# Kernel tuning notes

Hardware: AMD Instinct MI355X
Metric: run time of the kernel (lower is better)

Reference implementation:

```python
import jax, jax.numpy as jnp
import numpy as np

B, T, D = 2, 2048, 1024
NH, NKV, HD = 16, 4, 64
ROPE = 16  # partial RoPE dims (first 16 of 64)
HALF = ROPE // 2


def apply_rope(x, cos, sin):
    # x: (B, nH, T, HD); rotate first ROPE dims, pass the rest through
    x1 = x[..., :HALF]
    x2 = x[..., HALF:ROPE]
    xp = x[..., ROPE:]
    c = cos[None, None, :, :]  # (1,1,T,HALF)
    s = sin[None, None, :, :]
    return jnp.concatenate([x1 * c - x2 * s, x1 * s + x2 * c, xp], axis=-1)


def setup_inputs() -> dict:
    key = jax.random.key(0)
    k0, k1, k2 = jax.random.split(key, 3)
    x = jax.random.normal(k0, (B, T, D), dtype=jnp.float32)
    # RoPE tables for the rotated sub-dimension (half = ROPE//2 = 8)
    inv_freq = 1.0 / (10000.0 ** (jnp.arange(HALF, dtype=jnp.float32) / HALF))
    ang = jnp.arange(T, dtype=jnp.float32)[:, None] * inv_freq[None, :]
    cos = jnp.cos(ang)
    sin = jnp.sin(ang)
    attn_mask = jnp.tril(jnp.ones((T, T), dtype=bool))  # causal
    w_qkv = jax.random.normal(k1, ((NH + 2 * NKV) * HD, D), dtype=jnp.float32) * (D ** -0.5)
    w_out = jax.random.normal(k2, (D, D), dtype=jnp.float32) * (D ** -0.5)
    q_scale = jnp.full((NH, 1), 1.5, dtype=jnp.float32)
    k_scale = jnp.full((NKV, 1), 1.5, dtype=jnp.float32)
    return {"x": x, "cos": cos, "sin": sin, "attn_mask": attn_mask,
            "w_qkv": w_qkv, "w_out": w_out, "q_scale": q_scale, "k_scale": k_scale}


def reference(x, cos, sin, attn_mask, w_qkv, w_out, q_scale, k_scale):
    Bx, Tx, C = x.shape
    groups = NH // NKV
    qkv = x @ w_qkv.T  # (B,T,(NH+2*NKV)*HD)
    q, k, v = jnp.split(qkv, [NH * HD, (NH + NKV) * HD], axis=-1)
    q = q.reshape(Bx, Tx, NH, HD).transpose(0, 2, 1, 3)    # (B,NH,T,HD)
    k = k.reshape(Bx, Tx, NKV, HD).transpose(0, 2, 1, 3)   # (B,NKV,T,HD)
    v = v.reshape(Bx, Tx, NKV, HD).transpose(0, 2, 1, 3)
    # per-head qk gain scaling
    q = q * q_scale[None, :, :, None]  # (1,NH,1,1)
    k = k * k_scale[None, :, :, None]
    # partial RoPE on q and k
    q = apply_rope(q, cos[:Tx], sin[:Tx])
    k = apply_rope(k, cos[:Tx], sin[:Tx])
    # GQA expand (repeat_interleave along heads)
    ke = jnp.repeat(k, groups, axis=1)  # (B,NH,T,HD)
    ve = jnp.repeat(v, groups, axis=1)
    # scaled dot-product attention with causal mask
    scores = jnp.einsum('bhqd,bhkd->bhqk', q, ke) * (HD ** -0.5)
    scores = jnp.where(attn_mask[None, None], scores, -jnp.inf)
    probs = jax.nn.softmax(scores, axis=-1)
    ao = jnp.einsum('bhqk,bhkd->bhqd', probs, ve)  # (B,NH,T,HD)
    # xsa: subtract self-component along the (shared) kv value direction
    ao_r = ao.reshape(Bx, NKV, groups, Tx, HD)
    vv = v[:, :, None]  # (B,NKV,1,T,HD), broadcasts over groups
    dots = jnp.sum(ao_r * vv, axis=-1, keepdims=True)
    norm = jnp.maximum(jnp.sum(vv * vv, axis=-1, keepdims=True), 1e-8)
    ao = (ao_r - (dots / norm) * vv).reshape(Bx, NH, Tx, HD)
    out = ao.transpose(0, 2, 1, 3).reshape(Bx, Tx, C) @ w_out.T
    return out
```

## Files before the change

kernel.cpp:

```cpp
#include <hip/hip_runtime.h>
#include <hip/hip_bf16.h>

#define NB 2
#define NT 2048
#define ND 1024
#define NHEADS 16
#define NKVH 4
#define HDIM 64
#define QKVD 1536

typedef __attribute__((ext_vector_type(8))) short short8;
typedef __attribute__((ext_vector_type(4))) float floatx4;

#if defined(__has_builtin)
#  if __has_builtin(__builtin_amdgcn_global_load_lds)
#    define HAS_GLL 1
#  endif
#endif
#ifndef HAS_GLL
#  define HAS_GLL 0
#endif

__device__ __forceinline__ void gll16(const void* g, void* l, int lane) {
#if HAS_GLL
  (void)lane;
  __builtin_amdgcn_global_load_lds(
      (const __attribute__((address_space(1))) unsigned int*)g,
      (__attribute__((address_space(3))) unsigned int*)l, 16, 0, 0);
#else
  *(short8*)((short*)l) = *(const short8*)g;
#endif
}

__device__ __forceinline__ unsigned short f2bf(float f) {
  union { float f; unsigned int u; } cv; cv.f = f;
  unsigned int u = cv.u;
  u += 0x7fffu + ((u >> 16) & 1u);
  return (unsigned short)(u >> 16);
}
__device__ __forceinline__ float bf2f(unsigned short u) {
  union { unsigned int u; float f; } cv; cv.u = ((unsigned int)u) << 16; return cv.f;
}

__global__ __launch_bounds__(256) void cvt_bf16(const float* __restrict__ in,
                                                unsigned short* __restrict__ out,
                                                int n4) {
  int i = blockIdx.x * 256 + threadIdx.x;
  if (i < n4) {
    float4 v = ((const float4*)in)[i];
    ushort4 o;
    o.x = f2bf(v.x); o.y = f2bf(v.y); o.z = f2bf(v.z); o.w = f2bf(v.w);
    ((ushort4*)out)[i] = o;
  }
}

__global__ __launch_bounds__(256) void gemm_lds(
    const unsigned short* __restrict__ A,
    const unsigned short* __restrict__ Bm,
    float* __restrict__ C, int M, int N, int K)
{
  __shared__ __align__(16) short As[2][128][32];
  __shared__ __align__(16) short Bs[2][128][32];

  const int tid = threadIdx.x;
  const int wid = tid >> 6, lane = tid & 63;
  const int quad = lane >> 4, l16 = lane & 15;
  const int wm = (wid >> 1) * 64, wn = (wid & 1) * 64;
  const int m0 = blockIdx.x * 128, n0 = blockIdx.y * 128;

  const int r0 = tid >> 2;
  const int lc = ((tid & 3) ^ (r0 & 3)) * 8;

  const unsigned short* ag0 = A  + (size_t)(m0 + r0) * K + lc;
  const unsigned short* ag1 = ag0 + (size_t)64 * K;
  const unsigned short* bg0 = Bm + (size_t)(n0 + r0) * K + lc;
  const unsigned short* bg1 = bg0 + (size_t)64 * K;

  short* asb = &As[0][0][0];
  short* bsb = &Bs[0][0][0];
  const int lofs = (HAS_GLL ? wid * 512 : tid * 8);

  const int cs = (quad ^ (l16 & 3)) * 8;

  floatx4 acc[4][4] = {};

  gll16(ag0, asb + lofs, lane);
  gll16(ag1, asb + 2048 + lofs, lane);
  gll16(bg0, bsb + lofs, lane);
  gll16(bg1, bsb + 2048 + lofs, lane);

  const int NIT = K / 32;
  for (int it = 0; it < NIT; it++) {
    __syncthreads();
    const int bi = it & 1, bn = bi ^ 1;
    if (it + 1 < NIT) {
      const int k = (it + 1) * 32;
      gll16(ag0 + k, asb + bn * 4096 + lofs, lane);
      gll16(ag1 + k, asb + bn * 4096 + 2048 + lofs, lane);
      gll16(bg0 + k, bsb + bn * 4096 + lofs, lane);
      gll16(bg1 + k, bsb + bn * 4096 + 2048 + lofs, lane);
    }

    short8 af[4], bf[4];
#pragma unroll
    for (int mi = 0; mi < 4; mi++) af[mi] = *(const short8*)&As[bi][wm + mi * 16 + l16][cs];
#pragma unroll
    for (int ni = 0; ni < 4; ni++) bf[ni] = *(const short8*)&Bs[bi][wn + ni * 16 + l16][cs];
#pragma unroll
    for (int mi = 0; mi < 4; mi++)
#pragma unroll
      for (int ni = 0; ni < 4; ni++)
        acc[mi][ni] = __builtin_amdgcn_mfma_f32_16x16x32_bf16(af[mi], bf[ni], acc[mi][ni], 0, 0, 0);
  }

#pragma unroll
  for (int mi = 0; mi < 4; mi++)
#pragma unroll
    for (int ni = 0; ni < 4; ni++)
#pragma unroll
      for (int r = 0; r < 4; r++) {
        int m = m0 + wm + mi * 16 + quad * 4 + r;
        int n = n0 + wn + ni * 16 + l16;
        C[(size_t)m * N + n] = acc[mi][ni][r];
      }
}

__global__ __launch_bounds__(256) void rope_pack(
    const float* __restrict__ qkv,
    const float* __restrict__ cosT, const float* __restrict__ sinT,
    const float* __restrict__ q_scale, const float* __restrict__ k_scale,
    unsigned short* __restrict__ qb, unsigned short* __restrict__ kb)
{
  const int b  = blockIdx.z;
  const int hh = blockIdx.y * 4 + (threadIdx.x >> 6);
  const int d  = threadIdx.x & 63;

  float scale; int soff; unsigned short* dbase;
  if (hh < NHEADS) {
    scale = q_scale[hh] * (0.125f * 1.44269504088896f);
    soff = hh * HDIM;
    dbase = qb + ((size_t)(b * NHEADS + hh) * NT) * HDIM;
  } else {
    int kvh = hh - NHEADS;
    scale = k_scale[kvh];
    soff = NHEADS * HDIM + kvh * HDIM;
    dbase = kb + ((size_t)(b * NKVH + kvh) * NT) * HDIM;
  }

  for (int i = 0; i < 8; i++) {
    const int t = blockIdx.x * 8 + i;
    const float* src = qkv + ((size_t)(b * NT + t)) * QKVD + soff;
    float out;
    if (d < 8) {
      float x1 = src[d], x2 = src[d + 8];
      float c = cosT[t * 8 + d], s = sinT[t * 8 + d];
      out = (x1 * c - x2 * s) * scale;
    } else if (d < 16) {
      float x1 = src[d - 8], x2 = src[d];
      float c = cosT[t * 8 + d - 8], s = sinT[t * 8 + d - 8];
      out = (x1 * s + x2 * c) * scale;
    } else {
      out = src[d] * scale;
    }
    dbase[(size_t)t * HDIM + d] = f2bf(out);
  }
}

__global__ __launch_bounds__(256) void vT(const float* __restrict__ qkv,
                                          unsigned short* __restrict__ vtb)
{
  const int tt  = blockIdx.x;
  const int kvh = blockIdx.y;
  const int b   = blockIdx.z;
  const int tid = threadIdx.x;

  __shared__ float tile[64][65];

  {
    const int tl = tid >> 2, d0 = (tid & 3) * 16;
    const float* src = qkv + ((size_t)(b * NT + tt * 64 + tl)) * QKVD
                       + (NHEADS + NKVH) * HDIM + kvh * HDIM + d0;
#pragma unroll
    for (int j = 0; j < 16; j += 4) {
      float4 v = *(const float4*)(src + j);
      tile[tl][d0 + j + 0] = v.x; tile[tl][d0 + j + 1] = v.y;
      tile[tl][d0 + j + 2] = v.z; tile[tl][d0 + j + 3] = v.w;
    }
  }
  __syncthreads();
  {
    const int dd = tid >> 2, t0 = (tid & 3) * 16;
    unsigned short* dst = vtb + ((size_t)((b * NKVH + kvh) * HDIM + dd)) * NT + tt * 64 + t0;
#pragma unroll
    for (int j = 0; j < 16; j++) dst[j] = f2bf(tile[t0 + j][dd]);
  }
}

__global__ __launch_bounds__(256) void fattn(
    const unsigned short* __restrict__ qb,
    const unsigned short* __restrict__ kb,
    const unsigned short* __restrict__ vtb,
    unsigned short* __restrict__ aob,
    float* __restrict__ pbuf)
{
  const int idx = blockIdx.x;
  const int h = blockIdx.y, b = blockIdx.z;
  const int kv = h >> 2;

  int qt, j0, cnt, chunk; bool direct;
  if (idx < 16) { qt = 16 + idx; j0 = 0; cnt = 16; chunk = 0; direct = false; }
  else {
    int rel = idx - 16, s = 16 - (rel >> 1);
    if ((rel & 1) == 0) { qt = s - 1;  j0 = 0;  cnt = s; chunk = 0; direct = true;  }
    else                { qt = s + 15; j0 = 16; cnt = s; chunk = 1; direct = false; }
  }

  const int tid = threadIdx.x;
  const int wid = tid >> 6, lane = tid & 63;
  const int quad = lane >> 4, l16 = lane & 15;
  const int hi8 = l16 >> 3, lo8 = l16 & 7;

  __shared__ __align__(16) short Ks[2][64][64];
  __shared__ __align__(16) short Vs[2][64][64];
  __shared__ __align__(16) short Ps[4][16][64];

  const unsigned short* qg = qb + ((size_t)((b * NHEADS + h) * NT + qt * 64)) * HDIM;
  const int qrow = wid * 16 + l16;
  short8 aq0 = *(const short8*)(qg + (size_t)qrow * HDIM + quad * 8);
  short8 aq1 = *(const short8*)(qg + (size_t)qrow * HDIM + 32 + quad * 8);

  const int sr  = tid >> 3;
  const int lck = ((tid & 7) ^ (sr & 7)) * 8;
  const unsigned short* kgp0 = kb  + ((size_t)((b * NKVH + kv) * NT) + sr) * HDIM + lck;
  const unsigned short* vgp0 = vtb + ((size_t)((b * NKVH + kv) * HDIM) + sr) * NT + lck;
  short* ksb = &Ks[0][0][0];
  short* vsb = &Vs[0][0][0];
  const int lofs = (HAS_GLL ? wid * 512 : tid * 8);

  const int cs0 = (quad ^ lo8) * 8;
  const int cs1 = cs0 ^ 32;

  int pwo[4][4];
#pragma unroll
  for (int r = 0; r < 4; r++) {
    const int row = quad * 4 + r;
#pragma unroll
    for (int nb = 0; nb < 4; nb++)
      pwo[r][nb] = wid * 1024 + row * 64 + (((nb * 2 + hi8) ^ (row & 7)) * 8) + lo8;
  }
  short* psf = &Ps[0][0][0];

  floatx4 acc_o[4] = {};
  float lsum[4] = {0.f, 0.f, 0.f, 0.f};

  {
    const unsigned short* kg = kgp0 + (size_t)j0 * 64 * HDIM;
    const unsigned short* vg = vgp0 + j0 * 64;
    gll16(kg, ksb + lofs, lane);
    gll16(kg + 32 * HDIM, ksb + 2048 + lofs, lane);
    gll16(vg, vsb + lofs, lane);
    gll16(vg + (size_t)32 * NT, vsb + 2048 + lofs, lane);
  }

  for (int i = 0; i < cnt; i++) {
    const int jt = j0 + i;
    __syncthreads();
    const int bi = i & 1, bn = bi ^ 1;
    if (i + 1 < cnt) {
      const unsigned short* kg = kgp0 + (size_t)(jt + 1) * 64 * HDIM;
      const unsigned short* vg = vgp0 + (jt + 1) * 64;
      gll16(kg, ksb + bn * 4096 + lofs, lane);
      gll16(kg + 32 * HDIM, ksb + bn * 4096 + 2048 + lofs, lane);
      gll16(vg, vsb + bn * 4096 + lofs, lane);
      gll16(vg + (size_t)32 * NT, vsb + bn * 4096 + 2048 + lofs, lane);
    }

    floatx4 s[4] = {};
#pragma unroll
    for (int nb = 0; nb < 4; nb++) {
      short8 bk0 = *(const short8*)&Ks[bi][nb * 16 + l16][cs0];
      short8 bk1 = *(const short8*)&Ks[bi][nb * 16 + l16][cs1];
      s[nb] = __builtin_amdgcn_mfma_f32_16x16x32_bf16(aq0, bk0, s[nb], 0, 0, 0);
      s[nb] = __builtin_amdgcn_mfma_f32_16x16x32_bf16(aq1, bk1, s[nb], 0, 0, 0);
    }

    if (jt == qt) {
#pragma unroll
      for (int nb = 0; nb < 4; nb++) {
        int col = nb * 16 + l16;
#pragma unroll
        for (int r = 0; r < 4; r++)
          if (col > wid * 16 + quad * 4 + r) s[nb][r] = -INFINITY;
      }
    }

#pragma unroll
    for (int r = 0; r < 4; r++) {
#pragma unroll
      for (int nb = 0; nb < 4; nb++) {
        float p = __builtin_amdgcn_exp2f(s[nb][r]);
        lsum[r] += p;
        psf[pwo[r][nb]] = (short)(__float_as_uint(p) >> 16);
      }
    }

    short8 ap0 = *(const short8*)&Ps[wid][l16][cs0];
    short8 ap1 = *(const short8*)&Ps[wid][l16][cs1];
#pragma unroll
    for (int nb = 0; nb < 4; nb++) {
      short8 bv0 = *(const short8*)&Vs[bi][nb * 16 + l16][cs0];
      short8 bv1 = *(const short8*)&Vs[bi][nb * 16 + l16][cs1];
      acc_o[nb] = __builtin_amdgcn_mfma_f32_16x16x32_bf16(ap0, bv0, acc_o[nb], 0, 0, 0);
      acc_o[nb] = __builtin_amdgcn_mfma_f32_16x16x32_bf16(ap1, bv1, acc_o[nb], 0, 0, 0);
    }
  }

  const int bl = (cnt - 1) & 1;

  if (direct) {
#pragma unroll
    for (int r = 0; r < 4; r++) {
      float ls = lsum[r];
#pragma unroll
      for (int off = 1; off < 16; off <<= 1) ls += __shfl_xor(ls, off);
      const float invl = 1.f / ls;

      const int rowl = wid * 16 + quad * 4 + r;
      const int vcol = ((rowl >> 3) ^ lo8) * 8 + (rowl & 7);
      float vd[4], dot = 0.f, vv = 0.f;
#pragma unroll
      for (int nb = 0; nb < 4; nb++) {
        vd[nb] = bf2f((unsigned short)Vs[bl][nb * 16 + l16][vcol]);
        dot += acc_o[nb][r] * invl * vd[nb];
        vv  += vd[nb] * vd[nb];
      }
#pragma unroll
      for (int off = 1; off < 16; off <<= 1) {
        dot += __shfl_xor(dot, off);
        vv  += __shfl_xor(vv, off);
      }
      const float coef = dot / fmaxf(vv, 1e-8f);
      unsigned short* dst = aob + ((size_t)(b * NT + qt * 64 + rowl)) * ND + h * HDIM + l16;
#pragma unroll
      for (int nb = 0; nb < 4; nb++)
        dst[nb * 16] = f2bf(acc_o[nb][r] * invl - coef * vd[nb]);
    }
  } else {
    const int slot = ((b * NHEADS + h) * 16 + (qt - 16)) * 2 + chunk;
    float* pO = pbuf + (size_t)slot * 4160;
    float* pl = pO + 4096;
#pragma unroll
    for (int r = 0; r < 4; r++) {
      float ls = lsum[r];
#pragma unroll
      for (int off = 1; off < 16; off <<= 1) ls += __shfl_xor(ls, off);
      const int rowl = wid * 16 + quad * 4 + r;
      if (l16 == 0) pl[rowl] = ls;
#pragma unroll
      for (int nb = 0; nb < 4; nb++)
        pO[rowl * 64 + nb * 16 + l16] = acc_o[nb][r];
    }
  }
}

__global__ __launch_bounds__(256) void redn(
    const float* __restrict__ pbuf,
    const unsigned short* __restrict__ vtb,
    unsigned short* __restrict__ aob)
{
  const int qt = 16 + blockIdx.x;
  const int h = blockIdx.y, b = blockIdx.z;
  const int kv = h >> 2;
  const int tid = threadIdx.x;

  const int slot0 = ((b * NHEADS + h) * 16 + blockIdx.x) * 2;
  const float* O0 = pbuf + (size_t)slot0 * 4160;
  const float* O1 = O0 + 4160;
  const float* l0 = O0 + 4096;
  const float* l1 = O1 + 4096;

  __shared__ short vt[64][66];

  {
    const int d = tid >> 2, tq = (tid & 3) * 16;
    const unsigned short* src = vtb + ((size_t)((b * NKVH + kv) * HDIM + d)) * NT + qt * 64 + tq;
    short8 v0 = *(const short8*)src;
    short8 v1 = *(const short8*)(src + 8);
    *(short8*)&vt[d][tq] = v0;
    *(short8*)&vt[d][tq + 8] = v1;
  }
  __syncthreads();

  const int row = tid >> 2, dq = tid & 3;
  const float invl = 1.f / (l0[row] + l1[row]);

  float o[16], vd[16];
  float dot = 0.f, vv = 0.f;
#pragma unroll
  for (int j = 0; j < 16; j++) {
    const int d = dq * 16 + j;
    float ov = (O0[row * 64 + d] + O1[row * 64 + d]) * invl;
    float v  = bf2f((unsigned short)vt[d][row]);
    o[j] = ov; vd[j] = v;
    dot += ov * v; vv += v * v;
  }
  dot += __shfl_xor(dot, 1); dot += __shfl_xor(dot, 2);
  vv  += __shfl_xor(vv, 1);  vv  += __shfl_xor(vv, 2);
  const float coef = dot / fmaxf(vv, 1e-8f);

  unsigned short* dst = aob + ((size_t)(b * NT + qt * 64 + row)) * ND + h * HDIM + dq * 16;
  ushort4 w0, w1, w2, w3;
  w0.x = f2bf(o[0] - coef * vd[0]);  w0.y = f2bf(o[1] - coef * vd[1]);
  w0.z = f2bf(o[2] - coef * vd[2]);  w0.w = f2bf(o[3] - coef * vd[3]);
  w1.x = f2bf(o[4] - coef * vd[4]);  w1.y = f2bf(o[5] - coef * vd[5]);
  w1.z = f2bf(o[6] - coef * vd[6]);  w1.w = f2bf(o[7] - coef * vd[7]);
  w2.x = f2bf(o[8] - coef * vd[8]);  w2.y = f2bf(o[9] - coef * vd[9]);
  w2.z = f2bf(o[10] - coef * vd[10]); w2.w = f2bf(o[11] - coef * vd[11]);
  w3.x = f2bf(o[12] - coef * vd[12]); w3.y = f2bf(o[13] - coef * vd[13]);
  w3.z = f2bf(o[14] - coef * vd[14]); w3.w = f2bf(o[15] - coef * vd[15]);
  ((ushort4*)dst)[0] = w0; ((ushort4*)dst)[1] = w1;
  ((ushort4*)dst)[2] = w2; ((ushort4*)dst)[3] = w3;
}

extern "C" void kernel_launch(void* const* d_in, const int* in_sizes, int n_in,
                              void* d_out, int out_size, void* d_ws, size_t ws_size,
                              hipStream_t stream) {
  const float* x       = (const float*)d_in[0];
  const float* cosT    = (const float*)d_in[1];
  const float* sinT    = (const float*)d_in[2];
  const float* w_qkv   = (const float*)d_in[4];
  const float* w_out   = (const float*)d_in[5];
  const float* q_scale = (const float*)d_in[6];
  const float* k_scale = (const float*)d_in[7];
  float* out = (float*)d_out;

  char* ws = (char*)d_ws;
  unsigned short* xb    = (unsigned short*)ws;
  unsigned short* qb    = xb;
  unsigned short* wqkvb = (unsigned short*)(ws + 8388608);
  unsigned short* kb    = wqkvb;
  unsigned short* woutb = (unsigned short*)(ws + 11534336);
  float*          qkv   = (float*)(ws + 13631488);
  float*          pbuf  = qkv;
  unsigned short* vtb   = (unsigned short*)(ws + 38797312);
  unsigned short* aob   = (unsigned short*)(ws + 40894464);

  cvt_bf16<<<(NB * NT * ND / 4 + 255) / 256, 256, 0, stream>>>(x, xb, NB * NT * ND / 4);
  cvt_bf16<<<(QKVD * ND / 4 + 255) / 256, 256, 0, stream>>>(w_qkv, wqkvb, QKVD * ND / 4);
  cvt_bf16<<<(ND * ND / 4 + 255) / 256, 256, 0, stream>>>(w_out, woutb, ND * ND / 4);

  gemm_lds<<<dim3(NB * NT / 128, QKVD / 128), 256, 0, stream>>>(
      xb, wqkvb, qkv, NB * NT, QKVD, ND);

  rope_pack<<<dim3(NT / 8, 5, NB), 256, 0, stream>>>(qkv, cosT, sinT, q_scale, k_scale, qb, kb);
  vT<<<dim3(NT / 64, NKVH, NB), 256, 0, stream>>>(qkv, vtb);

  fattn<<<dim3(48, NHEADS, NB), 256, 0, stream>>>(qb, kb, vtb, aob, pbuf);
  redn<<<dim3(16, NHEADS, NB), 256, 0, stream>>>(pbuf, vtb, aob);

  gemm_lds<<<dim3(NB * NT / 128, ND / 128), 256, 0, stream>>>(
      aob, woutb, out, NB * NT, ND, ND);
}
```

Measured before the change: 216.2 us.

## Fuse RoPE, scaling, bf16 pack and V transpose into QKV GEMM epilogue

The three fp32-to-bf16 conversion launches become a single kernel, and the QKV GEMM now applies the head scales, partial RoPE (exchanging rotate pairs through a lane shuffle), bf16 conversion and the V transpose directly in its epilogue. This drops the fp32 qkv intermediate round trip through memory and removes the rope_pack and vT launches. The workspace layout is reorganised to match. The cost is an epilogue with scattered 2-byte stores for Q/K and strided ushort4 stores for V^T, which may coalesce worse than the old dedicated kernels.

Result: faster. 195.2 us (-9.7%).

```diff
diff --git a/kernel.cpp b/kernel.cpp
--- a/kernel.cpp
+++ b/kernel.cpp
@@ -42,29 +42,41 @@
   union { unsigned int u; float f; } cv; cv.u = ((unsigned int)u) << 16; return cv.f;
 }
 
-__global__ __launch_bounds__(256) void cvt_bf16(const float* __restrict__ in,
-                                                unsigned short* __restrict__ out,
-                                                int n4) {
+#define N4_X   1048576
+#define N4_WQ   393216
+#define N4_WO   262144
+__global__ __launch_bounds__(256) void cvt_all(
+    const float* __restrict__ x, const float* __restrict__ wq,
+    const float* __restrict__ wo,
+    unsigned short* __restrict__ xb, unsigned short* __restrict__ wqb,
+    unsigned short* __restrict__ wob) {
   int i = blockIdx.x * 256 + threadIdx.x;
-  if (i < n4) {
-    float4 v = ((const float4*)in)[i];
-    ushort4 o;
-    o.x = f2bf(v.x); o.y = f2bf(v.y); o.z = f2bf(v.z); o.w = f2bf(v.w);
-    ((ushort4*)out)[i] = o;
-  }
-}
-
-__global__ __launch_bounds__(256) void gemm_lds(
+  const float* src; unsigned short* dst; int j;
+  if (i < N4_X)              { src = x;  dst = xb;  j = i; }
+  else if (i < N4_X + N4_WQ) { src = wq; dst = wqb; j = i - N4_X; }
+  else                       { src = wo; dst = wob; j = i - N4_X - N4_WQ; }
+  float4 v = ((const float4*)src)[j];
+  ushort4 o;
+  o.x = f2bf(v.x); o.y = f2bf(v.y); o.z = f2bf(v.z); o.w = f2bf(v.w);
+  ((ushort4*)dst)[j] = o;
+}
+
+__global__ __launch_bounds__(256) void gemm_qkv(
     const unsigned short* __restrict__ A,
     const unsigned short* __restrict__ Bm,
-    float* __restrict__ C, int M, int N, int K)
+    const float* __restrict__ cosT, const float* __restrict__ sinT,
+    const float* __restrict__ q_scale, const float* __restrict__ k_scale,
+    unsigned short* __restrict__ qb, unsigned short* __restrict__ kb,
+    unsigned short* __restrict__ vtb)
 {
+  const int M = NB * NT, N = QKVD, K = ND;
   __shared__ __align__(16) short As[2][128][32];
   __shared__ __align__(16) short Bs[2][128][32];
 
   const int tid = threadIdx.x;
   const int wid = tid >> 6, lane = tid & 63;
   const int quad = lane >> 4, l16 = lane & 15;
+  const int lo8 = l16 & 7;
   const int wm = (wid >> 1) * 64, wn = (wid & 1) * 64;
   const int m0 = blockIdx.x * 128, n0 = blockIdx.y * 128;
 
@@ -79,7 +91,6 @@
   short* asb = &As[0][0][0];
   short* bsb = &Bs[0][0][0];
   const int lofs = (HAS_GLL ? wid * 512 : tid * 8);
-
   const int cs = (quad ^ (l16 & 3)) * 8;
 
   floatx4 acc[4][4] = {};
@@ -100,7 +111,107 @@
       gll16(bg0 + k, bsb + bn * 4096 + lofs, lane);
       gll16(bg1 + k, bsb + bn * 4096 + 2048 + lofs, lane);
     }
-
+    short8 af[4], bf[4];
+#pragma unroll
+    for (int mi = 0; mi < 4; mi++) af[mi] = *(const short8*)&As[bi][wm + mi * 16 + l16][cs];
+#pragma unroll
+    for (int ni = 0; ni < 4; ni++) bf[ni] = *(const short8*)&Bs[bi][wn + ni * 16 + l16][cs];
+#pragma unroll
+    for (int mi = 0; mi < 4; mi++)
+#pragma unroll
+      for (int ni = 0; ni < 4; ni++)
+        acc[mi][ni] = __builtin_amdgcn_mfma_f32_16x16x32_bf16(af[mi], bf[ni], acc[mi][ni], 0, 0, 0);
+  }
+
+  const int hh = blockIdx.y * 2 + (wid & 1);
+
+  if (hh >= NHEADS + NKVH) {
+    const int kvh = hh - (NHEADS + NKVH);
+#pragma unroll
+    for (int mi = 0; mi < 4; mi++) {
+      const int mrow = m0 + wm + mi * 16 + quad * 4;
+      const int bb = mrow >> 11, tt = mrow & (NT - 1);
+#pragma unroll
+      for (int ni = 0; ni < 4; ni++) {
+        const int d = ni * 16 + l16;
+        ushort4 w;
+        w.x = f2bf(acc[mi][ni][0]); w.y = f2bf(acc[mi][ni][1]);
+        w.z = f2bf(acc[mi][ni][2]); w.w = f2bf(acc[mi][ni][3]);
+        *(ushort4*)(vtb + ((size_t)((bb * NKVH + kvh) * HDIM + d)) * NT + tt) = w;
+      }
+    }
+  } else {
+    float scl; unsigned short* dst0; int hloc;
+    if (hh < NHEADS) { scl = q_scale[hh] * (0.125f * 1.44269504088896f); hloc = hh; dst0 = qb; }
+    else             { scl = k_scale[hh - NHEADS];                        hloc = hh - NHEADS; dst0 = kb; }
+    const int nh = (hh < NHEADS) ? NHEADS : NKVH;
+#pragma unroll
+    for (int mi = 0; mi < 4; mi++) {
+#pragma unroll
+      for (int r = 0; r < 4; r++) {
+        const int mrow = m0 + wm + mi * 16 + quad * 4 + r;
+        const int bb = mrow >> 11, tt = mrow & (NT - 1);
+        unsigned short* drow = dst0 + ((size_t)((bb * nh + hloc) * NT + tt)) * HDIM;
+
+        const float own = acc[mi][0][r];
+        const float oth = __shfl_xor(own, 8);
+        const float c = cosT[tt * 8 + lo8], s = sinT[tt * 8 + lo8];
+        const float roped = (l16 < 8) ? (own * c - oth * s)
+                                      : (oth * s + own * c);
+        drow[l16] = f2bf(roped * scl);
+#pragma unroll
+        for (int ni = 1; ni < 4; ni++)
+          drow[ni * 16 + l16] = f2bf(acc[mi][ni][r] * scl);
+      }
+    }
+  }
+}
+
+__global__ __launch_bounds__(256) void gemm_lds(
+    const unsigned short* __restrict__ A,
+    const unsigned short* __restrict__ Bm,
+    float* __restrict__ C, int M, int N, int K)
+{
+  __shared__ __align__(16) short As[2][128][32];
+  __shared__ __align__(16) short Bs[2][128][32];
+
+  const int tid = threadIdx.x;
+  const int wid = tid >> 6, lane = tid & 63;
+  const int quad = lane >> 4, l16 = lane & 15;
+  const int wm = (wid >> 1) * 64, wn = (wid & 1) * 64;
+  const int m0 = blockIdx.x * 128, n0 = blockIdx.y * 128;
+
+  const int r0 = tid >> 2;
+  const int lc = ((tid & 3) ^ (r0 & 3)) * 8;
+
+  const unsigned short* ag0 = A  + (size_t)(m0 + r0) * K + lc;
+  const unsigned short* ag1 = ag0 + (size_t)64 * K;
+  const unsigned short* bg0 = Bm + (size_t)(n0 + r0) * K + lc;
+  const unsigned short* bg1 = bg0 + (size_t)64 * K;
+
+  short* asb = &As[0][0][0];
+  short* bsb = &Bs[0][0][0];
+  const int lofs = (HAS_GLL ? wid * 512 : tid * 8);
+  const int cs = (quad ^ (l16 & 3)) * 8;
+
+  floatx4 acc[4][4] = {};
+
+  gll16(ag0, asb + lofs, lane);
+  gll16(ag1, asb + 2048 + lofs, lane);
+  gll16(bg0, bsb + lofs, lane);
+  gll16(bg1, bsb + 2048 + lofs, lane);
+
+  const int NIT = K / 32;
+  for (int it = 0; it < NIT; it++) {
+    __syncthreads();
+    const int bi = it & 1, bn = bi ^ 1;
+    if (it + 1 < NIT) {
+      const int k = (it + 1) * 32;
+      gll16(ag0 + k, asb + bn * 4096 + lofs, lane);
+      gll16(ag1 + k, asb + bn * 4096 + 2048 + lofs, lane);
+      gll16(bg0 + k, bsb + bn * 4096 + lofs, lane);
+      gll16(bg1 + k, bsb + bn * 4096 + 2048 + lofs, lane);
+    }
     short8 af[4], bf[4];
 #pragma unroll
     for (int mi = 0; mi < 4; mi++) af[mi] = *(const short8*)&As[bi][wm + mi * 16 + l16][cs];
@@ -123,77 +234,6 @@
         int n = n0 + wn + ni * 16 + l16;
         C[(size_t)m * N + n] = acc[mi][ni][r];
       }
-}
-
-__global__ __launch_bounds__(256) void rope_pack(
-    const float* __restrict__ qkv,
-    const float* __restrict__ cosT, const float* __restrict__ sinT,
-    const float* __restrict__ q_scale, const float* __restrict__ k_scale,
-    unsigned short* __restrict__ qb, unsigned short* __restrict__ kb)
-{
-  const int b  = blockIdx.z;
-  const int hh = blockIdx.y * 4 + (threadIdx.x >> 6);
-  const int d  = threadIdx.x & 63;
-
-  float scale; int soff; unsigned short* dbase;
-  if (hh < NHEADS) {
-    scale = q_scale[hh] * (0.125f * 1.44269504088896f);
-    soff = hh * HDIM;
-    dbase = qb + ((size_t)(b * NHEADS + hh) * NT) * HDIM;
-  } else {
-    int kvh = hh - NHEADS;
-    scale = k_scale[kvh];
-    soff = NHEADS * HDIM + kvh * HDIM;
-    dbase = kb + ((size_t)(b * NKVH + kvh) * NT) * HDIM;
-  }
-
-  for (int i = 0; i < 8; i++) {
-    const int t = blockIdx.x * 8 + i;
-    const float* src = qkv + ((size_t)(b * NT + t)) * QKVD + soff;
-    float out;
-    if (d < 8) {
-      float x1 = src[d], x2 = src[d + 8];
-      float c = cosT[t * 8 + d], s = sinT[t * 8 + d];
-      out = (x1 * c - x2 * s) * scale;
-    } else if (d < 16) {
-      float x1 = src[d - 8], x2 = src[d];
-      float c = cosT[t * 8 + d - 8], s = sinT[t * 8 + d - 8];
-      out = (x1 * s + x2 * c) * scale;
-    } else {
-      out = src[d] * scale;
-    }
-    dbase[(size_t)t * HDIM + d] = f2bf(out);
-  }
-}
-
-__global__ __launch_bounds__(256) void vT(const float* __restrict__ qkv,
-                                          unsigned short* __restrict__ vtb)
-{
-  const int tt  = blockIdx.x;
-  const int kvh = blockIdx.y;
-  const int b   = blockIdx.z;
-  const int tid = threadIdx.x;
-
-  __shared__ float tile[64][65];
-
-  {
-    const int tl = tid >> 2, d0 = (tid & 3) * 16;
-    const float* src = qkv + ((size_t)(b * NT + tt * 64 + tl)) * QKVD
-                       + (NHEADS + NKVH) * HDIM + kvh * HDIM + d0;
-#pragma unroll
-    for (int j = 0; j < 16; j += 4) {
-      float4 v = *(const float4*)(src + j);
-      tile[tl][d0 + j + 0] = v.x; tile[tl][d0 + j + 1] = v.y;
-      tile[tl][d0 + j + 2] = v.z; tile[tl][d0 + j + 3] = v.w;
-    }
-  }
-  __syncthreads();
-  {
-    const int dd = tid >> 2, t0 = (tid & 3) * 16;
-    unsigned short* dst = vtb + ((size_t)((b * NKVH + kvh) * HDIM + dd)) * NT + tt * 64 + t0;
-#pragma unroll
-    for (int j = 0; j < 16; j++) dst[j] = f2bf(tile[t0 + j][dd]);
-  }
 }
 
 __global__ __launch_bounds__(256) void fattn(
@@ -436,24 +476,19 @@
 
   char* ws = (char*)d_ws;
   unsigned short* xb    = (unsigned short*)ws;
-  unsigned short* qb    = xb;
   unsigned short* wqkvb = (unsigned short*)(ws + 8388608);
-  unsigned short* kb    = wqkvb;
-  unsigned short* woutb = (unsigned short*)(ws + 11534336);
-  float*          qkv   = (float*)(ws + 13631488);
-  float*          pbuf  = qkv;
-  unsigned short* vtb   = (unsigned short*)(ws + 38797312);
-  unsigned short* aob   = (unsigned short*)(ws + 40894464);
-
-  cvt_bf16<<<(NB * NT * ND / 4 + 255) / 256, 256, 0, stream>>>(x, xb, NB * NT * ND / 4);
-  cvt_bf16<<<(QKVD * ND / 4 + 255) / 256, 256, 0, stream>>>(w_qkv, wqkvb, QKVD * ND / 4);
-  cvt_bf16<<<(ND * ND / 4 + 255) / 256, 256, 0, stream>>>(w_out, woutb, ND * ND / 4);
-
-  gemm_lds<<<dim3(NB * NT / 128, QKVD / 128), 256, 0, stream>>>(
-      xb, wqkvb, qkv, NB * NT, QKVD, ND);
-
-  rope_pack<<<dim3(NT / 8, 5, NB), 256, 0, stream>>>(qkv, cosT, sinT, q_scale, k_scale, qb, kb);
-  vT<<<dim3(NT / 64, NKVH, NB), 256, 0, stream>>>(qkv, vtb);
+  float*          pbuf  = (float*)ws;
+  unsigned short* woutb = (unsigned short*)(ws + 17825792);
+  unsigned short* qb    = (unsigned short*)(ws + 19922944);
+  unsigned short* kb    = (unsigned short*)(ws + 28311552);
+  unsigned short* vtb   = (unsigned short*)(ws + 30408704);
+  unsigned short* aob   = (unsigned short*)(ws + 32505856);
+
+  cvt_all<<<(N4_X + N4_WQ + N4_WO) / 256, 256, 0, stream>>>(
+      x, w_qkv, w_out, xb, wqkvb, woutb);
+
+  gemm_qkv<<<dim3(NB * NT / 128, QKVD / 128), 256, 0, stream>>>(
+      xb, wqkvb, cosT, sinT, q_scale, k_scale, qb, kb, vtb);
 
   fattn<<<dim3(48, NHEADS, NB), 256, 0, stream>>>(qb, kb, vtb, aob, pbuf);
   redn<<<dim3(16, NHEADS, NB), 256, 0, stream>>>(pbuf, vtb, aob);
```
